# Kernel optimization log

Measured on AMD Instinct MI355X. Metric: run time of the kernel, lower is better.

Reference implementation:

```python
import jax, jax.numpy as jnp
import numpy as np

# --- dims (match init_kwargs) ---
H = 2048      # hidden_dim
NH = 16       # num_heads
QL = 1536     # q_latent_dim
KVL = 512     # kv_latent_dim
QR = 64       # q_rope_dim (== k_rope_dim)
QN = 128      # q_nope_dim
KR = 64       # k_rope_dim
KN = 128      # k_nope_dim
VD = 128      # v_dim
B, S = 1, 2048
BASE = 10000.0
EPS = 1e-6


def rms_norm(x, w, eps=EPS):
    xf = x.astype(jnp.float32)
    var = jnp.mean(xf * xf, axis=-1, keepdims=True)
    return w * (xf * jax.lax.rsqrt(var + eps)).astype(x.dtype)


def rope_cos_sin(seq_len, dim, base=BASE):
    inv_freq = 1.0 / (base ** (jnp.arange(0, dim, 2, dtype=jnp.float32) / dim))
    t = jnp.arange(seq_len, dtype=jnp.float32)
    freqs = jnp.outer(t, inv_freq)
    emb = jnp.concatenate([freqs, freqs], axis=-1)  # [S, dim]
    return jnp.cos(emb), jnp.sin(emb)


def rotate_half(x):
    d = x.shape[-1] // 2
    return jnp.concatenate([-x[..., d:], x[..., :d]], axis=-1)


def apply_rotary_pos_emb(q, k, cos, sin, position_ids):
    # cos/sin: [S, d]; position_ids: [B, S] -> [B, 1, S, d]
    cos = cos[position_ids][:, None]
    sin = sin[position_ids][:, None]

    def interleave(x):  # matches view(b,h,s,d//2,2).transpose(4,3).reshape
        b, h, s, d = x.shape
        return x.reshape(b, h, s, d // 2, 2).transpose(0, 1, 2, 4, 3).reshape(b, h, s, d)

    q = interleave(q)
    k = interleave(k)
    return q * cos + rotate_half(q) * sin, k * cos + rotate_half(k) * sin


def setup_inputs() -> dict:
    key = jax.random.key(0)
    ks = jax.random.split(key, 8)
    sc = 0.02
    hidden_states = jax.random.normal(ks[0], (B, S, H), dtype=jnp.float32)
    position_ids = jnp.broadcast_to(jnp.arange(S, dtype=jnp.int32), (B, S))
    attn_mask = jnp.tril(jnp.ones((S, S), dtype=jnp.int32))[None, None]  # causal, [1,1,S,S]
    return {
        "hidden_states": hidden_states,
        "position_ids": position_ids,
        "attn_mask": attn_mask,
        "q_down_w": jax.random.normal(ks[1], (QL, H), jnp.float32) * sc,
        "kv_down_w": jax.random.normal(ks[2], (KVL + KR, H), jnp.float32) * sc,
        "q_up_w": jax.random.normal(ks[3], (NH * (QN + QR), QL), jnp.float32) * sc,
        "k_up_w": jax.random.normal(ks[4], (NH * (KN + VD), KVL), jnp.float32) * sc,
        "o_w": jax.random.normal(ks[5], (H, NH * VD), jnp.float32) * sc,
        "q_norm_w": jnp.ones((QL,), jnp.float32),
        "kv_norm_w": jnp.ones((KVL + KR,), jnp.float32),
    }


def reference(hidden_states, position_ids, attn_mask, q_down_w, kv_down_w,
              q_up_w, k_up_w, o_w, q_norm_w, kv_norm_w):
    bsz, seq_len, _ = hidden_states.shape

    # --- query path: down-proj -> RMSNorm -> up-proj ---
    latent_cq = rms_norm(hidden_states @ q_down_w.T, q_norm_w)        # [B,S,QL]
    q = latent_cq @ q_up_w.T                                          # [B,S,NH*(QN+QR)]
    q = q.reshape(bsz, seq_len, NH, QN + QR).transpose(0, 2, 1, 3)    # [B,NH,S,QN+QR]
    q_nope, q_pe = q[..., :QN], q[..., QN:]

    # --- kv path: down-proj -> RMSNorm -> split latent / shared k_pe ---
    compressed_kv = rms_norm(hidden_states @ kv_down_w.T, kv_norm_w)  # [B,S,KVL+KR]
    latent_ckv, k_pe = compressed_kv[..., :KVL], compressed_kv[..., KVL:]
    kv = latent_ckv @ k_up_w.T                                        # [B,S,NH*(KN+VD)]
    kv = kv.reshape(bsz, seq_len, NH, KN + VD).transpose(0, 2, 1, 3)  # [B,NH,S,KN+VD]
    k_nope, value = kv[..., :KN], kv[..., KN:]

    # --- partial RoPE on rotary sub-dims ---
    cos, sin = rope_cos_sin(seq_len, QR)
    k_pe = k_pe[:, None]                                              # [B,1,S,KR] shared across heads
    q_rope, k_rope = apply_rotary_pos_emb(q_pe, k_pe, cos, sin, position_ids)
    k_rope = jnp.broadcast_to(k_rope, (bsz, NH, seq_len, KR))

    query = jnp.concatenate([q_rope, q_nope], axis=-1)                # [B,NH,S,QR+QN]
    key = jnp.concatenate([k_rope, k_nope], axis=-1)                  # [B,NH,S,KR+KN]

    # --- explicit attention (no 1/sqrt(d) scale, matching the source) ---
    attn_weights = jnp.einsum('bhqd,bhkd->bhqk', query, key)
    attn_weights = jnp.where(attn_mask == 0, -jnp.inf, attn_weights)
    attn_weights = jax.nn.softmax(attn_weights, axis=-1)
    attn_output = jnp.einsum('bhqk,bhkd->bhqd', attn_weights, value)
    attn_output = attn_output.transpose(0, 2, 1, 3).reshape(bsz, seq_len, NH * VD)
    attn_output = attn_output @ o_w.T                                 # [B,S,H]
    return attn_weights, attn_output
```

## Files before the change

### kernel.cpp

```cpp
#include <hip/hip_runtime.h>
#include <cstdint>
#include <cmath>

typedef _Float16 f16;
using f16x8 = __attribute__((ext_vector_type(8))) _Float16;
using f16x4 = __attribute__((ext_vector_type(4))) _Float16;
using f32x4 = __attribute__((ext_vector_type(4))) float;

#define NHEAD 16
#define SEQ   2048
#define KS    2
#define NEG_INF -3.0e38f

static __device__ __forceinline__ f32x4 mfma16(f16x8 a, f16x8 b, f32x4 c) {
    return __builtin_amdgcn_mfma_f32_16x16x32_f16(a, b, c, 0, 0, 0);
}

static __device__ __forceinline__ void gload16(const void* gp, void* lp) {
    __builtin_amdgcn_global_load_lds(
        (const __attribute__((address_space(1))) unsigned int*)gp,
        (__attribute__((address_space(3))) unsigned int*)lp, 16, 0, 0);
}

__global__ __launch_bounds__(256) void k_cvt_all(
    const float* __restrict__ hsrc, const float* __restrict__ qdw, const float* __restrict__ kvdw,
    const float* __restrict__ quw, const float* __restrict__ kuw, const float* __restrict__ ow,
    f16* __restrict__ h16, f16* __restrict__ dw16, f16* __restrict__ quw16,
    f16* __restrict__ kuw16, f16* __restrict__ ow16)
{
    constexpr int C1 = 1048576;
    constexpr int C2 = C1 + 786432;
    constexpr int C3 = C2 + 327680;
    constexpr int C4 = C3 + 1179648;
    constexpr int C5 = C4 + 524288;
    int chunk = blockIdx.x * 256 + threadIdx.x;
    const float* src; f16* dst; int off; int nvalid;
    if (chunk < C1)      { src = hsrc; dst = h16;  off = chunk;      nvalid = 4194304; }
    else if (chunk < C2) { src = qdw;  dst = dw16; off = chunk - C1; nvalid = 3145728; }
    else if (chunk < C3) { src = kvdw; dst = dw16 + 3145728; off = chunk - C2; nvalid = 1179648; }
    else if (chunk < C4) { src = quw;  dst = quw16; off = chunk - C3; nvalid = 4718592; }
    else if (chunk < C5) { src = kuw;  dst = kuw16; off = chunk - C4; nvalid = 2097152; }
    else                 { src = ow;   dst = ow16;  off = chunk - C5; nvalid = 4194304; }
    int i = off * 4;
    f16x4 o;
#pragma unroll
    for (int k = 0; k < 4; k++) {
        int idx = i + k;
        float v = (idx < nvalid) ? src[idx] : 0.f;
        o[k] = (f16)v;
    }
    *(f16x4*)&dst[i] = o;
}

__global__ __launch_bounds__(256) void k_rope_table(float* __restrict__ cs)
{
    int idx = blockIdx.x * 256 + threadIdx.x;
    int t = idx >> 5;
    int j = idx & 31;
    float invf = (float)pow(10000.0, -(double)j / 32.0);
    float ang  = (float)t * invf;
    cs[t * 64 + j]      = (float)cos((double)ang);
    cs[t * 64 + 32 + j] = (float)sin((double)ang);
}

template <typename OutT, bool NT>
static __device__ __forceinline__ void gemm_body(const f16* __restrict__ A, const f16* __restrict__ B,
                                                 OutT* __restrict__ C, int K, int ldc,
                                                 int m0, int n0, int k0, int k1,
                                                 f16* As, f16* Bs)
{
    const int tid  = threadIdx.x;
    const int lane = tid & 63;
    const int wv   = tid >> 6;
    const int l15  = lane & 15;
    const int lg   = lane >> 4;
    const int wm   = (wv >> 1) * 64;
    const int wn   = (wv & 1) * 64;

    f32x4 acc[4][4] = {};

    const int r0  = tid >> 2;
    const int kc0 = (tid & 3) * 8;

    f16* asb0 = &As[(size_t)wv * 512];
    f16* asb1 = &As[2048 + (size_t)wv * 512];
    f16* bsb0 = &Bs[(size_t)wv * 512];
    f16* bsb1 = &Bs[2048 + (size_t)wv * 512];
    const f16* ap = &A[(size_t)(m0 + r0) * K + kc0];
    const f16* bp = &B[(size_t)(n0 + r0) * K + kc0];

    for (int kt = k0; kt < k1; kt += 32) {
        __syncthreads();
        gload16(ap + kt, asb0);
        gload16(ap + (size_t)64 * K + kt, asb1);
        gload16(bp + kt, bsb0);
        gload16(bp + (size_t)64 * K + kt, bsb1);
        __syncthreads();
        f16x8 af[4], bf[4];
#pragma unroll
        for (int i = 0; i < 4; i++)
            af[i] = *(const f16x8*)&As[(wm + i * 16 + l15) * 32 + lg * 8];
#pragma unroll
        for (int i = 0; i < 4; i++)
            bf[i] = *(const f16x8*)&Bs[(wn + i * 16 + l15) * 32 + lg * 8];
#pragma unroll
        for (int i = 0; i < 4; i++)
#pragma unroll
            for (int j = 0; j < 4; j++)
                acc[i][j] = mfma16(af[i], bf[j], acc[i][j]);
    }
#pragma unroll
    for (int i = 0; i < 4; i++) {
#pragma unroll
        for (int j = 0; j < 4; j++) {
            const int row = m0 + wm + i * 16 + lg * 4;
            const int col = n0 + wn + j * 16 + l15;
#pragma unroll
            for (int r = 0; r < 4; r++) {
                if constexpr (NT)
                    __builtin_nontemporal_store((OutT)acc[i][j][r], &C[(size_t)(row + r) * ldc + col]);
                else
                    C[(size_t)(row + r) * ldc + col] = (OutT)acc[i][j][r];
            }
        }
    }
}

template <typename OutT, bool NT, int SPLITK>
__global__ __launch_bounds__(256) void k_gemm(const f16* __restrict__ A, const f16* __restrict__ B,
                                              OutT* __restrict__ C, int K, int ldc, size_t zstride)
{
    __shared__ __align__(16) f16 lds[8192];
    const int ks   = (SPLITK > 1) ? (int)blockIdx.z : 0;
    const int ksub = K / SPLITK;
    gemm_body<OutT, NT>(A, B, C + (size_t)ks * zstride, K, ldc,
                        blockIdx.y * 128, blockIdx.x * 128, ks * ksub, ks * ksub + ksub,
                        lds, lds + 4096);
}

__global__ __launch_bounds__(256) void k_up_fused(const f16* __restrict__ cq, const f16* __restrict__ quw,
                                                  f16* __restrict__ q_all,
                                                  const f16* __restrict__ lat, const f16* __restrict__ kuw,
                                                  f16* __restrict__ kv_all)
{
    __shared__ __align__(16) f16 lds[8192];
    if (blockIdx.x < 24)
        gemm_body<f16, false>(cq, quw, q_all, 1536, 3072,
                              blockIdx.y * 128, blockIdx.x * 128, 0, 1536, lds, lds + 4096);
    else
        gemm_body<f16, false>(lat, kuw, kv_all, 512, 4096,
                              blockIdx.y * 128, (blockIdx.x - 24) * 128, 0, 512, lds, lds + 4096);
}

__global__ __launch_bounds__(256) void k_add2f(const float* __restrict__ p, float* __restrict__ out)
{
    size_t i = ((size_t)blockIdx.x * 256 + threadIdx.x) * 4;
    f32x4 a = *(const f32x4*)&p[i];
    f32x4 b = *(const f32x4*)&p[(size_t)2048 * 2048 + i];
    __builtin_nontemporal_store(a + b, (f32x4*)&out[i]);
}

__global__ __launch_bounds__(256) void k_rms_both(const float* __restrict__ P0, const float* __restrict__ P1,
                                                  const float* __restrict__ wq, const float* __restrict__ wkv,
                                                  f16* __restrict__ cq, f16* __restrict__ lat,
                                                  f16* __restrict__ kro, const float* __restrict__ cs)
{
    const int row = blockIdx.x, tid = threadIdx.x;
    const float* a = &P0[(size_t)row * 2176];
    const float* b = &P1[(size_t)row * 2176];
    float ssq = 0.f, ssk = 0.f;
    for (int c = tid; c < 1536; c += 256) { float v = a[c] + b[c]; ssq += v * v; }
    for (int c = 1536 + tid; c < 2112; c += 256) { float v = a[c] + b[c]; ssk += v * v; }
#pragma unroll
    for (int off = 32; off > 0; off >>= 1) {
        ssq += __shfl_xor(ssq, off);
        ssk += __shfl_xor(ssk, off);
    }
    __shared__ float part[4][2];
    if ((tid & 63) == 0) { part[tid >> 6][0] = ssq; part[tid >> 6][1] = ssk; }
    __syncthreads();
    float totq = part[0][0] + part[1][0] + part[2][0] + part[3][0];
    float totk = part[0][1] + part[1][1] + part[2][1] + part[3][1];
    float scq = 1.f / sqrtf(totq / 1536.f + 1e-6f);
    float sck = 1.f / sqrtf(totk / 576.f + 1e-6f);
    for (int c = tid; c < 1536; c += 256)
        cq[(size_t)row * 1536 + c] = (f16)(wq[c] * (a[c] + b[c]) * scq);
    for (int c = tid; c < 512; c += 256)
        lat[(size_t)row * 512 + c] = (f16)(wkv[c] * (a[1536 + c] + b[1536 + c]) * sck);
    if (tid < 32) {
        int j = tid;
        float va = wkv[512 + 2 * j] * (a[2048 + 2 * j] + b[2048 + 2 * j]) * sck;
        float vb = wkv[512 + 2 * j + 1] * (a[2048 + 2 * j + 1] + b[2048 + 2 * j + 1]) * sck;
        float cv = cs[row * 64 + j], sv = cs[row * 64 + 32 + j];
        kro[row * 64 + j]      = (f16)(va * cv - vb * sv);
        kro[row * 64 + 32 + j] = (f16)(vb * cv + va * sv);
    }
}

__global__ __launch_bounds__(256) void k_asm_q(const f16* __restrict__ q_all, const float* __restrict__ cs,
                                               f16* __restrict__ Qf)
{
    size_t idx = (size_t)blockIdx.x * 256 + threadIdx.x;
    if (idx >= (size_t)16 * 2048 * 192) return;
    int d = (int)(idx % 192);
    size_t hs = idx / 192;
    int s = (int)(hs % 2048);
    int h = (int)(hs / 2048);
    const f16* qrow = &q_all[(size_t)s * 3072 + h * 192];
    float v;
    if (d < 64) {
        int j = d & 31;
        float a = (float)qrow[128 + 2 * j], b = (float)qrow[128 + 2 * j + 1];
        float cv = cs[s * 64 + j], sv = cs[s * 64 + 32 + j];
        v = (d < 32) ? (a * cv - b * sv) : (b * cv + a * sv);
    } else {
        v = (float)qrow[d - 64];
    }
    Qf[idx] = (f16)v;
}

__global__ __launch_bounds__(256) void k_asm_kv(const f16* __restrict__ kv_all,
                                                f16* __restrict__ Knope,
                                                f16* __restrict__ Vt)
{
    __shared__ __align__(16) f16 Vs[128][136];
    const int s0 = blockIdx.x * 128;
    const int h  = blockIdx.y;
    const int tid = threadIdx.x;

#pragma unroll
    for (int i = 0; i < 16; i++) {
        const int c = tid + 256 * i;
        const int s_loc = c >> 5;
        const int g = c & 31;
        f16x8 v = *(const f16x8*)&kv_all[(size_t)(s0 + s_loc) * 4096 + h * 256 + g * 8];
        if (g < 16) {
            *(f16x8*)&Knope[((size_t)h * 2048 + s0 + s_loc) * 128 + g * 8] = v;
        } else {
            const int d0 = (g - 16) * 8;
#pragma unroll
            for (int k = 0; k < 8; k++) Vs[d0 + k][s_loc] = v[k];
        }
    }
    __syncthreads();
#pragma unroll
    for (int i = 0; i < 8; i++) {
        const int c = tid + 256 * i;
        const int d = c >> 4;
        const int gs = c & 15;
        f16x8 v = *(const f16x8*)&Vs[d][gs * 8];
        *(f16x8*)&Vt[((size_t)h * 128 + d) * 2048 + s0 + gs * 8] = v;
    }
}

__global__ __launch_bounds__(256) void k_stats(
    const f16* __restrict__ Qf, const f16* __restrict__ Krope, const f16* __restrict__ Knope,
    float* __restrict__ mlpart)
{
    const int h  = blockIdx.z;
    const int ks = blockIdx.y;
    const int qt = blockIdx.x;
    const int q0 = qt * 64;
    const int tid = threadIdx.x;
    const int lane = tid & 63;
    const int wv = tid >> 6;
    const int l15 = lane & 15;
    const int lg  = lane >> 4;
    const int rowb = q0 + wv * 16;

    __shared__ __align__(16) f16 Ks_[64][200];

    f16x8 qf[6];
    {
        const f16* qbase = &Qf[((size_t)h * SEQ + rowb + l15) * 192];
#pragma unroll
        for (int kf = 0; kf < 6; kf++)
            qf[kf] = *(const f16x8*)&qbase[kf * 32 + lg * 8];
    }

    float m[4], l[4];
#pragma unroll
    for (int r = 0; r < 4; r++) { m[r] = NEG_INF; l[r] = 0.f; }

    const int srow = tid >> 2;
    const int sp4  = tid & 3;
    const f32x4 vzero = {0.f, 0.f, 0.f, 0.f};

    for (int t = ks; t <= qt; t += KS) {
        const int c0 = t * 64;
        __syncthreads();
#pragma unroll
        for (int i = 0; i < 6; i++) {
            const int p = sp4 + 4 * i;
            f16x8 v;
            if (p < 8) v = *(const f16x8*)&Krope[(size_t)(c0 + srow) * 64 + p * 8];
            else       v = *(const f16x8*)&Knope[((size_t)h * SEQ + c0 + srow) * 128 + (p - 8) * 8];
            *(f16x8*)&Ks_[srow][p * 8] = v;
        }
        __syncthreads();

        f32x4 s[4];
#pragma unroll
        for (int ni = 0; ni < 4; ni++) {
            s[ni] = vzero;
            const f16* kp = &Ks_[ni * 16 + l15][0];
#pragma unroll
            for (int kf = 0; kf < 6; kf++)
                s[ni] = mfma16(qf[kf], *(const f16x8*)&kp[kf * 32 + lg * 8], s[ni]);
        }

        float vmax[4] = {NEG_INF, NEG_INF, NEG_INF, NEG_INF};
#pragma unroll
        for (int ni = 0; ni < 4; ni++) {
            const int col = c0 + ni * 16 + l15;
#pragma unroll
            for (int r = 0; r < 4; r++) {
                const int row = rowb + lg * 4 + r;
                float v = (col <= row) ? s[ni][r] : NEG_INF;
                s[ni][r] = v;
                vmax[r] = fmaxf(vmax[r], v);
            }
        }
#pragma unroll
        for (int off = 1; off < 16; off <<= 1)
#pragma unroll
            for (int r = 0; r < 4; r++)
                vmax[r] = fmaxf(vmax[r], __shfl_xor(vmax[r], off));
#pragma unroll
        for (int r = 0; r < 4; r++) {
            const float nm = fmaxf(m[r], vmax[r]);
            float es = 0.f;
#pragma unroll
            for (int ni = 0; ni < 4; ni++) es += expf(s[ni][r] - nm);
#pragma unroll
            for (int off = 1; off < 16; off <<= 1) es += __shfl_xor(es, off);
            l[r] = l[r] * expf(m[r] - nm) + es;
            m[r] = nm;
        }
    }

    if (l15 == 0) {
#pragma unroll
        for (int r = 0; r < 4; r++) {
            const int rin = wv * 16 + lg * 4 + r;
            float* mp = &mlpart[((((size_t)h * 32 + qt) * KS + ks) * 64 + rin) * 2];
            mp[0] = m[r];
            mp[1] = l[r];
        }
    }
}

__global__ __launch_bounds__(256) void k_mlcomb(const float* __restrict__ mlpart,
                                                float* __restrict__ mlbuf)
{
    int idx = blockIdx.x * 256 + threadIdx.x;
    if (idx >= 16 * 2048) return;
    int h = idx >> 11, row = idx & 2047;
    int qt = row >> 6, rin = row & 63;
    float mm = NEG_INF;
    float mk[KS], lk[KS];
#pragma unroll
    for (int ks = 0; ks < KS; ks++) {
        const float* mp = &mlpart[((((size_t)h * 32 + qt) * KS + ks) * 64 + rin) * 2];
        mk[ks] = mp[0]; lk[ks] = mp[1];
        mm = fmaxf(mm, mk[ks]);
    }
    float ll = 0.f;
#pragma unroll
    for (int ks = 0; ks < KS; ks++) ll += lk[ks] * expf(mk[ks] - mm);
    mlbuf[(size_t)idx * 2]     = mm;
    mlbuf[(size_t)idx * 2 + 1] = 1.f / ll;
}

__global__ __launch_bounds__(256) void k_pv(
    const f16* __restrict__ Qf, const f16* __restrict__ Krope, const f16* __restrict__ Knope,
    const f16* __restrict__ Vt, const float* __restrict__ mlbuf,
    float* __restrict__ attnw,
    f16* __restrict__ Opart)
{
    const int h  = blockIdx.z;
    const int ks = blockIdx.y;
    const int qt = blockIdx.x;
    const int q0 = qt * 64;
    const int tid = threadIdx.x;
    const int lane = tid & 63;
    const int wv = tid >> 6;
    const int l15 = lane & 15;
    const int lg  = lane >> 4;
    const int rowb = q0 + wv * 16;

    __shared__ __align__(16) f16 Ks_[64][200];
    __shared__ __align__(16) f16 Vs[128][72];
    __shared__ __align__(16) f16 Plds[4][16][72];

    f16x8 qf[6];
    {
        const f16* qbase = &Qf[((size_t)h * SEQ + rowb + l15) * 192];
#pragma unroll
        for (int kf = 0; kf < 6; kf++)
            qf[kf] = *(const f16x8*)&qbase[kf * 32 + lg * 8];
    }

    float mr[4], rlr[4];
#pragma unroll
    for (int r = 0; r < 4; r++) {
        const int row = rowb + lg * 4 + r;
        mr[r]  = mlbuf[((size_t)h * SEQ + row) * 2];
        rlr[r] = mlbuf[((size_t)h * SEQ + row) * 2 + 1];
    }

    f32x4 o[8] = {};
    const f32x4 vzero = {0.f, 0.f, 0.f, 0.f};
    const int srow = tid >> 2;
    const int sp4  = tid & 3;

    for (int t = ks; t <= qt; t += KS) {
        const int c0 = t * 64;
        __syncthreads();
#pragma unroll
        for (int i = 0; i < 6; i++) {
            const int p = sp4 + 4 * i;
            f16x8 v;
            if (p < 8) v = *(const f16x8*)&Krope[(size_t)(c0 + srow) * 64 + p * 8];
            else       v = *(const f16x8*)&Knope[((size_t)h * SEQ + c0 + srow) * 128 + (p - 8) * 8];
            *(f16x8*)&Ks_[srow][p * 8] = v;
        }
#pragma unroll
        for (int i = 0; i < 4; i++) {
            const int c = tid + 256 * i;
            const int d = c >> 3, x = c & 7;
            *(f16x8*)&Vs[d][x * 8] = *(const f16x8*)&Vt[((size_t)h * 128 + d) * SEQ + c0 + x * 8];
        }
        __syncthreads();

        f32x4 s[4];
#pragma unroll
        for (int ni = 0; ni < 4; ni++) {
            s[ni] = vzero;
            const f16* kp = &Ks_[ni * 16 + l15][0];
#pragma unroll
            for (int kf = 0; kf < 6; kf++)
                s[ni] = mfma16(qf[kf], *(const f16x8*)&kp[kf * 32 + lg * 8], s[ni]);
        }

#pragma unroll
        for (int ni = 0; ni < 4; ni++) {
            const int col = c0 + ni * 16 + l15;
#pragma unroll
            for (int r = 0; r < 4; r++) {
                const int row = rowb + lg * 4 + r;
                float p = (col <= row) ? expf(s[ni][r] - mr[r]) * rlr[r] : 0.f;
                __builtin_nontemporal_store(p, &attnw[((size_t)h * SEQ + row) * SEQ + col]);
                Plds[wv][lg * 4 + r][ni * 16 + l15] = (f16)p;
            }
        }
        asm volatile("" ::: "memory");

        f16x8 pa0 = *(const f16x8*)&Plds[wv][l15][lg * 8];
        f16x8 pa1 = *(const f16x8*)&Plds[wv][l15][32 + lg * 8];
#pragma unroll
        for (int nd = 0; nd < 8; nd++) {
            const f16* vp = &Vs[nd * 16 + l15][lg * 8];
            o[nd] = mfma16(pa0, *(const f16x8*)&vp[0],  o[nd]);
            o[nd] = mfma16(pa1, *(const f16x8*)&vp[32], o[nd]);
        }
    }

#pragma unroll
    for (int nd = 0; nd < 8; nd++)
#pragma unroll
        for (int r = 0; r < 4; r++) {
            const int row = rowb + lg * 4 + r;
            Opart[((size_t)ks * SEQ + row) * 2048 + h * 128 + nd * 16 + l15] = (f16)o[nd][r];
        }

    if (ks == KS - 1) {
        const int cstart = q0 + 64;
        const int zc = SEQ - cstart;
        if (zc > 0) {
            const int nchunk = zc >> 2;
            for (int i = tid; i < 64 * nchunk; i += 256) {
                const int r  = i / nchunk;
                const int cc = (i - r * nchunk) << 2;
                __builtin_nontemporal_store(vzero,
                    (f32x4*)&attnw[((size_t)h * SEQ + q0 + r) * SEQ + cstart + cc]);
            }
        }
    }
}

__global__ __launch_bounds__(256) void k_ocomb(const f16* __restrict__ Opart, f16* __restrict__ Ohead)
{
    size_t i = ((size_t)blockIdx.x * 256 + threadIdx.x) * 8;
    f16x8 a = *(const f16x8*)&Opart[i];
    f16x8 b = *(const f16x8*)&Opart[(size_t)SEQ * 2048 + i];
    f16x8 o;
#pragma unroll
    for (int k = 0; k < 8; k++) o[k] = (f16)((float)a[k] + (float)b[k]);
    *(f16x8*)&Ohead[i] = o;
}

extern "C" void kernel_launch(void* const* d_in, const int* in_sizes, int n_in,
                              void* d_out, int out_size, void* d_ws, size_t ws_size,
                              hipStream_t stream)
{
    (void)in_sizes; (void)n_in; (void)out_size; (void)ws_size;
    const float* hidden    = (const float*)d_in[0];
    const float* q_down_w  = (const float*)d_in[3];
    const float* kv_down_w = (const float*)d_in[4];
    const float* q_up_w    = (const float*)d_in[5];
    const float* k_up_w    = (const float*)d_in[6];
    const float* o_w       = (const float*)d_in[7];
    const float* q_norm_w  = (const float*)d_in[8];
    const float* kv_norm_w = (const float*)d_in[9];

    float* attnw = (float*)d_out;
    float* outp  = attnw + (size_t)NHEAD * SEQ * SEQ;

    char* wp = (char*)d_ws;
    auto aws = [&](size_t bytes) { void* p = (void*)wp; wp += (bytes + 255) & ~(size_t)255; return p; };
    f16*  ow16  = (f16*)aws((size_t)2048 * 2048 * 2);
    f16*  Ohead = (f16*)aws((size_t)2048 * 2048 * 2);
    f16*  Qf    = (f16*)aws((size_t)16 * 2048 * 192 * 2);
    f16*  Knope = (f16*)aws((size_t)16 * 2048 * 128 * 2);
    f16*  Vt    = (f16*)aws((size_t)16 * 128 * 2048 * 2);
    f16*  Krope = (f16*)aws((size_t)2048 * 64 * 2);
    float* cs   = (float*)aws((size_t)2048 * 64 * 4);
    float* mlbuf  = (float*)aws((size_t)16 * 2048 * 2 * 4);
    float* mlpart = (float*)aws((size_t)16 * 32 * KS * 64 * 2 * 4);
    f16*  Opart   = (f16*)aws((size_t)KS * 2048 * 2048 * 2);
    float* opp    = (float*)Qf;

    char* sp = (char*)d_out;
    auto aso = [&](size_t bytes) { void* p = (void*)sp; sp += (bytes + 255) & ~(size_t)255; return p; };
    f16*  h16      = (f16*)aso((size_t)2048 * 2048 * 2);
    f16*  dw16     = (f16*)aso((size_t)2176 * 2048 * 2);
    f16*  quw16    = (f16*)aso((size_t)3072 * 1536 * 2);
    f16*  kuw16    = (f16*)aso((size_t)4096 * 512 * 2);
    float* down_part = (float*)aso((size_t)2 * 2048 * 2176 * 4);
    f16*  cq16     = (f16*)aso((size_t)2048 * 1536 * 2);
    f16*  latent16 = (f16*)aso((size_t)2048 * 512 * 2);
    f16*  q_all    = (f16*)aso((size_t)2048 * 3072 * 2);
    f16*  kv_all   = (f16*)aso((size_t)2048 * 4096 * 2);

    k_rope_table<<<dim3(256), dim3(256), 0, stream>>>(cs);

    k_cvt_all<<<dim3(19200), dim3(256), 0, stream>>>(
        hidden, q_down_w, kv_down_w, q_up_w, k_up_w, o_w,
        h16, dw16, quw16, kuw16, ow16);

    k_gemm<float, false, 2><<<dim3(17, 16, 2), dim3(256), 0, stream>>>(
        h16, dw16, down_part, 2048, 2176, (size_t)2048 * 2176);

    k_rms_both<<<dim3(2048), dim3(256), 0, stream>>>(
        down_part, down_part + (size_t)2048 * 2176, q_norm_w, kv_norm_w,
        cq16, latent16, Krope, cs);

    k_up_fused<<<dim3(56, 16), dim3(256), 0, stream>>>(cq16, quw16, q_all, latent16, kuw16, kv_all);

    k_asm_q<<<dim3((16 * 2048 * 192) / 256), dim3(256), 0, stream>>>(q_all, cs, Qf);
    k_asm_kv<<<dim3(16, 16), dim3(256), 0, stream>>>(kv_all, Knope, Vt);

    k_stats<<<dim3(32, KS, 16), dim3(256), 0, stream>>>(Qf, Krope, Knope, mlpart);
    k_mlcomb<<<dim3(128), dim3(256), 0, stream>>>(mlpart, mlbuf);
    k_pv<<<dim3(32, KS, 16), dim3(256), 0, stream>>>(Qf, Krope, Knope, Vt, mlbuf, attnw, Opart);
    k_ocomb<<<dim3(2048), dim3(256), 0, stream>>>(Opart, Ohead);

    k_gemm<float, false, 2><<<dim3(16, 16, 2), dim3(256), 0, stream>>>(
        Ohead, ow16, opp, 2048, 2048, (size_t)2048 * 2048);
    k_add2f<<<dim3(4096), dim3(256), 0, stream>>>(opp, outp);
}
```

Before: 381.6 us.

## Double-buffer GEMM and stats K tiles, raise stats split to four

The shared GEMM body now uses two LDS buffers per operand. It issues the next K-slice's global-to-LDS loads before computing on the current slice, which drops one barrier per iteration. k_stats also double-buffers its K tile through registers and LDS, and its key-split factor goes from 2 to 4 (KSS) to expose more parallelism, with k_mlcomb and mlpart resized to match. LDS use per block doubles, which may reduce occupancy, and the stats partials to combine double.

```diff
diff --git a/kernel.cpp b/kernel.cpp
--- a/kernel.cpp
+++ b/kernel.cpp
@@ -10,6 +10,7 @@
 #define NHEAD 16
 #define SEQ   2048
 #define KS    2
+#define KSS   4
 #define NEG_INF -3.0e38f
 
 static __device__ __forceinline__ f32x4 mfma16(f16x8 a, f16x8 b, f32x4 c) {
@@ -67,7 +68,7 @@
 static __device__ __forceinline__ void gemm_body(const f16* __restrict__ A, const f16* __restrict__ B,
                                                  OutT* __restrict__ C, int K, int ldc,
                                                  int m0, int n0, int k0, int k1,
-                                                 f16* As, f16* Bs)
+                                                 f16* __restrict__ lds)
 {
     const int tid  = threadIdx.x;
     const int lane = tid & 63;
@@ -81,33 +82,38 @@
 
     const int r0  = tid >> 2;
     const int kc0 = (tid & 3) * 8;
-
-    f16* asb0 = &As[(size_t)wv * 512];
-    f16* asb1 = &As[2048 + (size_t)wv * 512];
-    f16* bsb0 = &Bs[(size_t)wv * 512];
-    f16* bsb1 = &Bs[2048 + (size_t)wv * 512];
     const f16* ap = &A[(size_t)(m0 + r0) * K + kc0];
     const f16* bp = &B[(size_t)(n0 + r0) * K + kc0];
 
+    f16* As[2] = { lds,        lds + 4096 };
+    f16* Bs[2] = { lds + 8192, lds + 12288 };
+
+    auto stage = [&](int kt, int buf) {
+        gload16(ap + kt,                     As[buf] + wv * 512);
+        gload16(ap + (size_t)64 * K + kt,    As[buf] + 2048 + wv * 512);
+        gload16(bp + kt,                     Bs[buf] + wv * 512);
+        gload16(bp + (size_t)64 * K + kt,    Bs[buf] + 2048 + wv * 512);
+    };
+
+    stage(k0, 0);
+    __syncthreads();
+    int cur = 0;
     for (int kt = k0; kt < k1; kt += 32) {
-        __syncthreads();
-        gload16(ap + kt, asb0);
-        gload16(ap + (size_t)64 * K + kt, asb1);
-        gload16(bp + kt, bsb0);
-        gload16(bp + (size_t)64 * K + kt, bsb1);
-        __syncthreads();
+        if (kt + 32 < k1) stage(kt + 32, cur ^ 1);
         f16x8 af[4], bf[4];
 #pragma unroll
         for (int i = 0; i < 4; i++)
-            af[i] = *(const f16x8*)&As[(wm + i * 16 + l15) * 32 + lg * 8];
+            af[i] = *(const f16x8*)&As[cur][(wm + i * 16 + l15) * 32 + lg * 8];
 #pragma unroll
         for (int i = 0; i < 4; i++)
-            bf[i] = *(const f16x8*)&Bs[(wn + i * 16 + l15) * 32 + lg * 8];
+            bf[i] = *(const f16x8*)&Bs[cur][(wn + i * 16 + l15) * 32 + lg * 8];
 #pragma unroll
         for (int i = 0; i < 4; i++)
 #pragma unroll
             for (int j = 0; j < 4; j++)
                 acc[i][j] = mfma16(af[i], bf[j], acc[i][j]);
+        __syncthreads();
+        cur ^= 1;
     }
 #pragma unroll
     for (int i = 0; i < 4; i++) {
@@ -130,12 +136,11 @@
 __global__ __launch_bounds__(256) void k_gemm(const f16* __restrict__ A, const f16* __restrict__ B,
                                               OutT* __restrict__ C, int K, int ldc, size_t zstride)
 {
-    __shared__ __align__(16) f16 lds[8192];
+    __shared__ __align__(16) f16 lds[16384];
     const int ks   = (SPLITK > 1) ? (int)blockIdx.z : 0;
     const int ksub = K / SPLITK;
     gemm_body<OutT, NT>(A, B, C + (size_t)ks * zstride, K, ldc,
-                        blockIdx.y * 128, blockIdx.x * 128, ks * ksub, ks * ksub + ksub,
-                        lds, lds + 4096);
+                        blockIdx.y * 128, blockIdx.x * 128, ks * ksub, ks * ksub + ksub, lds);
 }
 
 __global__ __launch_bounds__(256) void k_up_fused(const f16* __restrict__ cq, const f16* __restrict__ quw,
@@ -143,13 +148,13 @@
                                                   const f16* __restrict__ lat, const f16* __restrict__ kuw,
                                                   f16* __restrict__ kv_all)
 {
-    __shared__ __align__(16) f16 lds[8192];
+    __shared__ __align__(16) f16 lds[16384];
     if (blockIdx.x < 24)
         gemm_body<f16, false>(cq, quw, q_all, 1536, 3072,
-                              blockIdx.y * 128, blockIdx.x * 128, 0, 1536, lds, lds + 4096);
+                              blockIdx.y * 128, blockIdx.x * 128, 0, 1536, lds);
     else
         gemm_body<f16, false>(lat, kuw, kv_all, 512, 4096,
-                              blockIdx.y * 128, (blockIdx.x - 24) * 128, 0, 512, lds, lds + 4096);
+                              blockIdx.y * 128, (blockIdx.x - 24) * 128, 0, 512, lds);
 }
 
 __global__ __launch_bounds__(256) void k_add2f(const float* __restrict__ p, float* __restrict__ out)
@@ -268,74 +273,95 @@
     const int lg  = lane >> 4;
     const int rowb = q0 + wv * 16;
 
-    __shared__ __align__(16) f16 Ks_[64][200];
-
-    f16x8 qf[6];
-    {
-        const f16* qbase = &Qf[((size_t)h * SEQ + rowb + l15) * 192];
-#pragma unroll
-        for (int kf = 0; kf < 6; kf++)
-            qf[kf] = *(const f16x8*)&qbase[kf * 32 + lg * 8];
-    }
+    __shared__ __align__(16) f16 Ks_[2][64][200];
 
     float m[4], l[4];
 #pragma unroll
     for (int r = 0; r < 4; r++) { m[r] = NEG_INF; l[r] = 0.f; }
 
-    const int srow = tid >> 2;
-    const int sp4  = tid & 3;
-    const f32x4 vzero = {0.f, 0.f, 0.f, 0.f};
-
-    for (int t = ks; t <= qt; t += KS) {
-        const int c0 = t * 64;
+    if (ks <= qt) {
+        f16x8 qf[6];
+        {
+            const f16* qbase = &Qf[((size_t)h * SEQ + rowb + l15) * 192];
+#pragma unroll
+            for (int kf = 0; kf < 6; kf++)
+                qf[kf] = *(const f16x8*)&qbase[kf * 32 + lg * 8];
+        }
+        const int srow = tid >> 2;
+        const int sp4  = tid & 3;
+        const f32x4 vzero = {0.f, 0.f, 0.f, 0.f};
+
+        auto loadK = [&](int c0, f16x8 (&v)[6]) {
+#pragma unroll
+            for (int i = 0; i < 6; i++) {
+                const int p = sp4 + 4 * i;
+                if (p < 8) v[i] = *(const f16x8*)&Krope[(size_t)(c0 + srow) * 64 + p * 8];
+                else       v[i] = *(const f16x8*)&Knope[((size_t)h * SEQ + c0 + srow) * 128 + (p - 8) * 8];
+            }
+        };
+        auto writeK = [&](f16x8 (&v)[6], int buf) {
+#pragma unroll
+            for (int i = 0; i < 6; i++) {
+                const int p = sp4 + 4 * i;
+                *(f16x8*)&Ks_[buf][srow][p * 8] = v[i];
+            }
+        };
+
+        {
+            f16x8 v0[6];
+            loadK(ks * 64, v0);
+            writeK(v0, 0);
+        }
         __syncthreads();
-#pragma unroll
-        for (int i = 0; i < 6; i++) {
-            const int p = sp4 + 4 * i;
-            f16x8 v;
-            if (p < 8) v = *(const f16x8*)&Krope[(size_t)(c0 + srow) * 64 + p * 8];
-            else       v = *(const f16x8*)&Knope[((size_t)h * SEQ + c0 + srow) * 128 + (p - 8) * 8];
-            *(f16x8*)&Ks_[srow][p * 8] = v;
-        }
-        __syncthreads();
-
-        f32x4 s[4];
-#pragma unroll
-        for (int ni = 0; ni < 4; ni++) {
-            s[ni] = vzero;
-            const f16* kp = &Ks_[ni * 16 + l15][0];
-#pragma unroll
-            for (int kf = 0; kf < 6; kf++)
-                s[ni] = mfma16(qf[kf], *(const f16x8*)&kp[kf * 32 + lg * 8], s[ni]);
-        }
-
-        float vmax[4] = {NEG_INF, NEG_INF, NEG_INF, NEG_INF};
-#pragma unroll
-        for (int ni = 0; ni < 4; ni++) {
-            const int col = c0 + ni * 16 + l15;
+        int cur = 0;
+        for (int t = ks; t <= qt; t += KSS) {
+            const int c0 = t * 64;
+            const bool hasNext = (t + KSS <= qt);
+            f16x8 vn[6];
+            if (hasNext) loadK((t + KSS) * 64, vn);
+
+            f32x4 s[4];
+#pragma unroll
+            for (int ni = 0; ni < 4; ni++) {
+                s[ni] = vzero;
+                const f16* kp = &Ks_[cur][ni * 16 + l15][0];
+#pragma unroll
+                for (int kf = 0; kf < 6; kf++)
+                    s[ni] = mfma16(qf[kf], *(const f16x8*)&kp[kf * 32 + lg * 8], s[ni]);
+            }
+
+            float vmax[4] = {NEG_INF, NEG_INF, NEG_INF, NEG_INF};
+#pragma unroll
+            for (int ni = 0; ni < 4; ni++) {
+                const int col = c0 + ni * 16 + l15;
+#pragma unroll
+                for (int r = 0; r < 4; r++) {
+                    const int row = rowb + lg * 4 + r;
+                    float v = (col <= row) ? s[ni][r] : NEG_INF;
+                    s[ni][r] = v;
+                    vmax[r] = fmaxf(vmax[r], v);
+                }
+            }
+#pragma unroll
+            for (int off = 1; off < 16; off <<= 1)
+#pragma unroll
+                for (int r = 0; r < 4; r++)
+                    vmax[r] = fmaxf(vmax[r], __shfl_xor(vmax[r], off));
 #pragma unroll
             for (int r = 0; r < 4; r++) {
-                const int row = rowb + lg * 4 + r;
-                float v = (col <= row) ? s[ni][r] : NEG_INF;
-                s[ni][r] = v;
-                vmax[r] = fmaxf(vmax[r], v);
-            }
-        }
-#pragma unroll
-        for (int off = 1; off < 16; off <<= 1)
-#pragma unroll
-            for (int r = 0; r < 4; r++)
-                vmax[r] = fmaxf(vmax[r], __shfl_xor(vmax[r], off));
-#pragma unroll
-        for (int r = 0; r < 4; r++) {
-            const float nm = fmaxf(m[r], vmax[r]);
-            float es = 0.f;
-#pragma unroll
-            for (int ni = 0; ni < 4; ni++) es += expf(s[ni][r] - nm);
-#pragma unroll
-            for (int off = 1; off < 16; off <<= 1) es += __shfl_xor(es, off);
-            l[r] = l[r] * expf(m[r] - nm) + es;
-            m[r] = nm;
+                const float nm = fmaxf(m[r], vmax[r]);
+                float es = 0.f;
+#pragma unroll
+                for (int ni = 0; ni < 4; ni++) es += expf(s[ni][r] - nm);
+#pragma unroll
+                for (int off = 1; off < 16; off <<= 1) es += __shfl_xor(es, off);
+                l[r] = l[r] * expf(m[r] - nm) + es;
+                m[r] = nm;
+            }
+
+            if (hasNext) writeK(vn, cur ^ 1);
+            __syncthreads();
+            cur ^= 1;
         }
     }
 
@@ -343,7 +369,7 @@
 #pragma unroll
         for (int r = 0; r < 4; r++) {
             const int rin = wv * 16 + lg * 4 + r;
-            float* mp = &mlpart[((((size_t)h * 32 + qt) * KS + ks) * 64 + rin) * 2];
+            float* mp = &mlpart[((((size_t)h * 32 + qt) * KSS + ks) * 64 + rin) * 2];
             mp[0] = m[r];
             mp[1] = l[r];
         }
@@ -358,16 +384,16 @@
     int h = idx >> 11, row = idx & 2047;
     int qt = row >> 6, rin = row & 63;
     float mm = NEG_INF;
-    float mk[KS], lk[KS];
-#pragma unroll
-    for (int ks = 0; ks < KS; ks++) {
-        const float* mp = &mlpart[((((size_t)h * 32 + qt) * KS + ks) * 64 + rin) * 2];
+    float mk[KSS], lk[KSS];
+#pragma unroll
+    for (int ks = 0; ks < KSS; ks++) {
+        const float* mp = &mlpart[((((size_t)h * 32 + qt) * KSS + ks) * 64 + rin) * 2];
         mk[ks] = mp[0]; lk[ks] = mp[1];
         mm = fmaxf(mm, mk[ks]);
     }
     float ll = 0.f;
 #pragma unroll
-    for (int ks = 0; ks < KS; ks++) ll += lk[ks] * expf(mk[ks] - mm);
+    for (int ks = 0; ks < KSS; ks++) ll += lk[ks] * expf(mk[ks] - mm);
     mlbuf[(size_t)idx * 2]     = mm;
     mlbuf[(size_t)idx * 2 + 1] = 1.f / ll;
 }
@@ -527,7 +553,7 @@
     f16*  Krope = (f16*)aws((size_t)2048 * 64 * 2);
     float* cs   = (float*)aws((size_t)2048 * 64 * 4);
     float* mlbuf  = (float*)aws((size_t)16 * 2048 * 2 * 4);
-    float* mlpart = (float*)aws((size_t)16 * 32 * KS * 64 * 2 * 4);
+    float* mlpart = (float*)aws((size_t)16 * 32 * KSS * 64 * 2 * 4);
     f16*  Opart   = (f16*)aws((size_t)KS * 2048 * 2048 * 2);
     float* opp    = (float*)Qf;
 
@@ -561,7 +587,7 @@
     k_asm_q<<<dim3((16 * 2048 * 192) / 256), dim3(256), 0, stream>>>(q_all, cs, Qf);
     k_asm_kv<<<dim3(16, 16), dim3(256), 0, stream>>>(kv_all, Knope, Vt);
 
-    k_stats<<<dim3(32, KS, 16), dim3(256), 0, stream>>>(Qf, Krope, Knope, mlpart);
+    k_stats<<<dim3(32, KSS, 16), dim3(256), 0, stream>>>(Qf, Krope, Knope, mlpart);
     k_mlcomb<<<dim3(128), dim3(256), 0, stream>>>(mlpart, mlbuf);
     k_pv<<<dim3(32, KS, 16), dim3(256), 0, stream>>>(Qf, Krope, Knope, Vt, mlbuf, attnw, Opart);
     k_ocomb<<<dim3(2048), dim3(256), 0, stream>>>(Opart, Ohead);
```

Result: slower. 398.0 us (+4.3%).
